# Kernel optimization log

Measured on AMD Instinct MI355X. Metric: run time of the kernel, lower is better.

## Reference

```python
import jax, jax.numpy as jnp
import numpy as np

B, Tp, Tq, D2 = 16, 4096, 512, 256  # D2 = 2*d


def setup_inputs() -> dict:
    key = jax.random.key(0)
    k1, k2, k3 = jax.random.split(key, 3)
    H = jax.random.normal(k1, (B, Tp, D2), dtype=jnp.float32)
    U = jax.random.normal(k2, (B, Tq, D2), dtype=jnp.float32)
    # learned weight (1, 6d, 1, 1) in the original -> flat [6d] vector here
    w = jax.random.normal(k3, (3 * D2,), dtype=jnp.float32) * (1.0 / np.sqrt(3 * D2))
    mask_p = jnp.ones((B, Tp), dtype=jnp.int32)
    mask_q = jnp.ones((B, Tq), dtype=jnp.int32)
    return {"H": H, "U": U, "w": w, "mask_p": mask_p, "mask_q": mask_q}


def _masked_softmax(x, m, axis):
    # e = mask * exp(mask * (x - max(x)));  matches the original custom softmax
    e = m * jnp.exp(m * (x - jnp.max(x, axis=axis, keepdims=True)))
    return e / jnp.sum(e, axis=axis, keepdims=True)


def reference(H, U, w, mask_p, mask_q):
    pm = mask_p.astype(jnp.float32)          # [B, Tp]
    qm = mask_q.astype(jnp.float32)          # [B, Tq]
    Hm = H * pm[:, :, None]                  # [B, Tp, 2d]
    Um = U * qm[:, :, None]                  # [B, Tq, 2d]
    d2 = H.shape[-1]
    w_h, w_u, w_hu = w[:d2], w[d2:2 * d2], w[2 * d2:]
    # Decomposed additive score: S[b,i,j] = w_h.H[b,i] + w_u.U[b,j] + sum_c w_hu[c]*H[b,i,c]*U[b,j,c]
    # (identical math to summing w * concat([h_tiled, u_tiled, hu]) over the 6d axis)
    S = (Hm @ w_h)[:, :, None] + (Um @ w_u)[:, None, :] \
        + jnp.einsum('bic,bjc->bij', Hm * w_hu, Um)      # [B, Tp, Tq]
    a = _masked_softmax(S, qm[:, None, :], axis=-1)       # [B, Tp, Tq]
    U_att = jnp.einsum('bij,bjc->bic', a, Um)             # [B, Tp, 2d]
    b = _masked_softmax(jnp.max(S, axis=-1), pm, axis=-1) # [B, Tp]
    h_att = jnp.einsum('bi,bic->bc', b, Hm)               # [B, 2d]
    G = jnp.concatenate([Hm, U_att, Hm * U_att, Hm * h_att[:, None, :]], axis=-1)
    return G * pm[:, :, None]                             # [B, Tp, 8d]
```

## Files before the change

### kernel.cpp

```cpp
#include <hip/hip_runtime.h>
#include <hip/hip_bf16.h>
#include <cstdint>

#define B_  16
#define TP  4096
#define TQ  512
#define D2_ 256
#define TI 64
#define TJ 32
#define NJT (TQ / TJ)
#define NFRAG 35
#define PPITCH 34

typedef _Float16 f16x8 __attribute__((ext_vector_type(8)));
typedef _Float16 f16x4 __attribute__((ext_vector_type(4)));
typedef float    f32x4 __attribute__((ext_vector_type(4)));

__device__ __forceinline__ _Float16* frag_ptr(float* G, int b, int jt, int f, int lane) {
  return (_Float16*)G + ((size_t)((b * NJT + jt) * NFRAG + f)) * 2048 + 1536 + lane * 8;
}
__device__ __forceinline__ float* phat_ptr(float* G, int b, int blk) {
  return G + (size_t)(9000 + b * 64 + blk) * 1024 + 768;
}

__device__ __forceinline__ void gload_lds16(const _Float16* g, _Float16* l) {
  __builtin_amdgcn_global_load_lds(
      (const __attribute__((address_space(1))) void*)g,
      (__attribute__((address_space(3))) void*)l, 16, 0, 0);
}

__global__ __launch_bounds__(256) void k_prep(const float* __restrict__ U,
                                              const float* __restrict__ w,
                                              const int* __restrict__ mq,
                                              float* __restrict__ G) {
  __shared__ _Float16 T[TJ][264];
  __shared__ float uds[TJ];
  __shared__ float qs[TJ];
  const int b = blockIdx.y, jt = blockIdx.x;
  const int tid = threadIdx.x, lane = tid & 63, wv = tid >> 6;
  const int l15 = lane & 15, g = lane >> 4;

  if (tid < TJ) qs[tid] = (float)mq[b * TQ + jt * TJ + tid];

#pragma unroll
  for (int it = 0; it < 8; ++it) {
    int chunk = it * 256 + tid;
    int r = chunk >> 6, c = (chunk & 63) * 4;
    int row = b * TQ + jt * TJ + r;
    float qmv = (float)mq[row];
    f32x4 u = *(const f32x4*)&U[(size_t)row * D2_ + c];
    f16x4 v;
    v[0] = (_Float16)(u.x * qmv); v[1] = (_Float16)(u.y * qmv);
    v[2] = (_Float16)(u.z * qmv); v[3] = (_Float16)(u.w * qmv);
    *(f16x4*)&T[r][c] = v;
  }
  __syncthreads();

  {
    int r = tid >> 3, s = tid & 7;
    float p = 0.f;
#pragma unroll
    for (int e = 0; e < 32; ++e) p += (float)T[r][s * 32 + e] * w[D2_ + s * 32 + e];
    p += __shfl_xor(p, 1); p += __shfl_xor(p, 2); p += __shfl_xor(p, 4);
    if (s == 0) uds[r] = p;
  }
  __syncthreads();

#pragma unroll
  for (int q = 0; q < 9; ++q) {
    int f = q * 4 + wv;
    if (f >= NFRAG) continue;
    f16x8 v;
#pragma unroll
    for (int e = 0; e < 8; ++e) v[e] = (_Float16)0.0f;
    if (f < 16) {
      int t = f >> 3, ks = f & 7;
      v = *(const f16x8*)&T[t * 16 + l15][ks * 32 + g * 8];
    } else if (f < 18) {
      int t = f - 16;
      if (g == 0) { v[0] = (_Float16)uds[t * 16 + l15]; v[1] = (_Float16)1.0f; }
    } else if (f < 34) {
      int n = f - 18;
#pragma unroll
      for (int e = 0; e < 8; ++e) v[e] = T[g * 8 + e][n * 16 + l15];
    } else {
#pragma unroll
      for (int e = 0; e < 8; ++e) v[e] = (_Float16)qs[g * 8 + e];
    }
    *(f16x8*)frag_ptr(G, b, jt, f, lane) = v;
  }
}

__global__ __launch_bounds__(512, 4) void k_main(
    const float* __restrict__ H, const float* __restrict__ w,
    const int* __restrict__ mp,
    float* __restrict__ mblk_g, float* __restrict__ lblk_g,
    float* __restrict__ G) {

  __shared__ char smem[80896];
  _Float16 (*Fbuf)[NFRAG][512]  = (_Float16(*)[NFRAG][512])smem;
  _Float16 (*Plds)[16][PPITCH]  = (_Float16(*)[16][PPITCH])(smem + 71680);
  float* mtmp = (float*)(smem + 80384);
  float* wrow = mtmp + 64;
  _Float16 (*Uatt)[264] = (_Float16(*)[264])smem;
  f32x4 (*Part)[64]     = (f32x4(*)[64])smem;

  const int b = blockIdx.y, bx = blockIdx.x, i0 = bx * TI;
  const int tid = threadIdx.x, lane = tid & 63, wv = tid >> 6;
  const int l15 = lane & 15, g = lane >> 4;
  const int pr = wv >> 1;
  const int h  = wv & 1;

  const _Float16* Gf = (const _Float16*)G;
  auto tilebase = [&](int jt) {
    return Gf + ((size_t)((b * NJT + jt) * NFRAG)) * 2048 + 1536 + (size_t)lane * 8;
  };

  {
    const _Float16* fb = tilebase(0);
#pragma unroll
    for (int q = 0; q < 5; ++q) {
      int f = q * 8 + wv;
      if (f < NFRAG) gload_lds16(fb + (size_t)f * 2048, &Fbuf[0][f][0]);
    }
  }

  const int rowg = i0 + pr * 16 + l15;
  const float* Hrow = H + ((size_t)b * TP + rowg) * D2_;
  const float pmr = (float)mp[b * TP + rowg];
  f16x8 afr[8];
  float hp = 0.f;
#pragma unroll
  for (int ks = 0; ks < 8; ++ks) {
    int c0 = ks * 32 + g * 8;
    f32x4 h0 = *(const f32x4*)&Hrow[c0];
    f32x4 h1 = *(const f32x4*)&Hrow[c0 + 4];
    f32x4 wh0 = *(const f32x4*)&w[c0];
    f32x4 wh1 = *(const f32x4*)&w[c0 + 4];
    f32x4 wu0 = *(const f32x4*)&w[2 * D2_ + c0];
    f32x4 wu1 = *(const f32x4*)&w[2 * D2_ + c0 + 4];
    h0 *= pmr; h1 *= pmr;
    f16x8 a;
    a[0] = (_Float16)(h0.x * wu0.x); a[1] = (_Float16)(h0.y * wu0.y);
    a[2] = (_Float16)(h0.z * wu0.z); a[3] = (_Float16)(h0.w * wu0.w);
    a[4] = (_Float16)(h1.x * wu1.x); a[5] = (_Float16)(h1.y * wu1.y);
    a[6] = (_Float16)(h1.z * wu1.z); a[7] = (_Float16)(h1.w * wu1.w);
    afr[ks] = a;
    hp += h0.x * wh0.x + h0.y * wh0.y + h0.z * wh0.z + h0.w * wh0.w
        + h1.x * wh1.x + h1.y * wh1.y + h1.z * wh1.z + h1.w * wh1.w;
  }
  hp += __shfl_xor(hp, 16);
  hp += __shfl_xor(hp, 32);
  f16x8 bext;
#pragma unroll
  for (int e = 0; e < 8; ++e) bext[e] = (_Float16)0.0f;
  if (g == 0) { bext[0] = (_Float16)1.0f; bext[1] = (_Float16)hp; }

  __syncthreads();

  f32x4 Oacc[8];
#pragma unroll
  for (int n = 0; n < 8; ++n) Oacc[n] = {0.f, 0.f, 0.f, 0.f};
  f32x4 Lacc = {0.f, 0.f, 0.f, 0.f};
  float m_run  = -1e30f;
  float m_true = -1e30f;

  int cur = 0;
  for (int jt = 0; jt < NJT; ++jt) {
    if (jt + 1 < NJT) {
      const _Float16* fb = tilebase(jt + 1);
#pragma unroll
      for (int q = 0; q < 5; ++q) {
        int f = q * 8 + wv;
        if (f < NFRAG) gload_lds16(fb + (size_t)f * 2048, &Fbuf[cur ^ 1][f][0]);
      }
    }

    f32x4 S0 = {0.f, 0.f, 0.f, 0.f}, S1 = {0.f, 0.f, 0.f, 0.f};
#pragma unroll
    for (int ks = 0; ks < 8; ++ks) {
      f16x8 a0 = *(const f16x8*)&Fbuf[cur][ks][lane * 8];
      f16x8 a1 = *(const f16x8*)&Fbuf[cur][8 + ks][lane * 8];
      S0 = __builtin_amdgcn_mfma_f32_16x16x32_f16(a0, afr[ks], S0, 0, 0, 0);
      S1 = __builtin_amdgcn_mfma_f32_16x16x32_f16(a1, afr[ks], S1, 0, 0, 0);
    }
    {
      f16x8 ax0 = *(const f16x8*)&Fbuf[cur][16][lane * 8];
      f16x8 ax1 = *(const f16x8*)&Fbuf[cur][17][lane * 8];
      S0 = __builtin_amdgcn_mfma_f32_16x16x32_f16(ax0, bext, S0, 0, 0, 0);
      S1 = __builtin_amdgcn_mfma_f32_16x16x32_f16(ax1, bext, S1, 0, 0, 0);
    }

    float lmax = fmaxf(fmaxf(fmaxf(S0[0], S0[1]), fmaxf(S0[2], S0[3])),
                       fmaxf(fmaxf(S1[0], S1[1]), fmaxf(S1[2], S1[3])));
    lmax = fmaxf(lmax, __shfl_xor(lmax, 16));
    lmax = fmaxf(lmax, __shfl_xor(lmax, 32));
    m_true = fmaxf(m_true, lmax);
    if (__any(lmax - m_run > 8.0f)) {
      float mn = fmaxf(m_run, lmax);
      float sc = __expf(m_run - mn);
      m_run = mn;
#pragma unroll
      for (int reg = 0; reg < 4; ++reg) {
        float scr = __shfl(sc, g * 4 + reg);
        Lacc[reg] *= scr;
#pragma unroll
        for (int n = 0; n < 8; ++n) Oacc[n][reg] *= scr;
      }
    }

    f16x4 ph0, ph1;
#pragma unroll
    for (int reg = 0; reg < 4; ++reg) {
      ph0[reg] = (_Float16)__expf(S0[reg] - m_run);
      ph1[reg] = (_Float16)__expf(S1[reg] - m_run);
    }
    *(f16x4*)&Plds[wv][l15][g * 4]      = ph0;
    *(f16x4*)&Plds[wv][l15][16 + g * 4] = ph1;
    f16x8 pa = *(const f16x8*)&Plds[wv][l15][g * 8];

    {
      f16x8 qmf = *(const f16x8*)&Fbuf[cur][34][lane * 8];
      Lacc = __builtin_amdgcn_mfma_f32_16x16x32_f16(pa, qmf, Lacc, 0, 0, 0);
    }
#pragma unroll
    for (int n = 0; n < 8; ++n) {
      f16x8 bu = *(const f16x8*)&Fbuf[cur][18 + h * 8 + n][lane * 8];
      Oacc[n] = __builtin_amdgcn_mfma_f32_16x16x32_f16(pa, bu, Oacc[n], 0, 0, 0);
    }

    __syncthreads();
    cur ^= 1;
  }

  if (h == 0 && g == 0) mtmp[pr * 16 + l15] = m_true;
  float inv_l[4];
#pragma unroll
  for (int reg = 0; reg < 4; ++reg) inv_l[reg] = 1.0f / Lacc[reg];
  __syncthreads();

  if (wv == 0) {
    float v = mtmp[lane];
#pragma unroll
    for (int o = 1; o < 64; o <<= 1) v = fmaxf(v, __shfl_xor(v, o));
    float m_blk = v;
    float pmv = (float)mp[b * TP + i0 + lane];
    float wr = pmv * __expf(mtmp[lane] - m_blk);
    wrow[lane] = wr;
    float ls = wr;
#pragma unroll
    for (int o = 1; o < 64; o <<= 1) ls += __shfl_xor(ls, o);
    if (lane == 0) { mblk_g[b * 64 + bx] = m_blk; lblk_g[b * 64 + bx] = ls; }
  }

#pragma unroll
  for (int n = 0; n < 8; ++n)
#pragma unroll
    for (int reg = 0; reg < 4; ++reg)
      Uatt[pr * 16 + g * 4 + reg][h * 128 + n * 16 + l15] =
          (_Float16)(Oacc[n][reg] * inv_l[reg]);
  __syncthreads();

  const int* pmb = mp + b * TP + i0;
  f32x4 acc = {0.f, 0.f, 0.f, 0.f};
#pragma unroll
  for (int it = 0; it < 8; ++it) {
    int idx4 = it * 512 + tid;
    int r = idx4 >> 6, c = (idx4 & 63) * 4;
    float pm = (float)pmb[r];
    f32x4 hv = *(const f32x4*)&H[((size_t)b * TP + i0 + r) * D2_ + c];
    hv *= pm;
    f16x4 u4 = *(const f16x4*)&Uatt[r][c];
    f32x4 u; u.x = (float)u4[0]; u.y = (float)u4[1]; u.z = (float)u4[2]; u.w = (float)u4[3];
    size_t ro = ((size_t)b * TP + i0 + r) * (4 * D2_);
    *(f32x4*)&G[ro + c] = hv;
    f32x4 up = u * pm;
    *(f32x4*)&G[ro + D2_ + c] = up;
    f32x4 hu; hu.x = hv.x * u.x; hu.y = hv.y * u.y; hu.z = hv.z * u.z; hu.w = hv.w * u.w;
    *(f32x4*)&G[ro + 2 * D2_ + c] = hu;
    acc += wrow[r] * hv;
  }

  __syncthreads();
  Part[wv][lane] = acc;
  __syncthreads();
  if (tid < 64) {
    f32x4 s = Part[0][tid];
#pragma unroll
    for (int k = 1; k < 8; ++k) s += Part[k][tid];
    *(f32x4*)&phat_ptr(G, b, bx)[tid * 4] = s;
  }
}

__global__ __launch_bounds__(256) void k_comb(const float* __restrict__ Gc,
    const float* __restrict__ mblk_g, const float* __restrict__ lblk_g,
    float* __restrict__ hatt) {
  int b = blockIdx.x, tid = threadIdx.x;
  __shared__ float sm[64], sl[64];
  if (tid < 64) { sm[tid] = mblk_g[b * 64 + tid]; sl[tid] = lblk_g[b * 64 + tid]; }
  __syncthreads();
  float M = -1e30f;
#pragma unroll
  for (int k = 0; k < 64; ++k) M = fmaxf(M, sm[k]);
  float L = 0.f;
#pragma unroll
  for (int k = 0; k < 64; ++k) L += __expf(sm[k] - M) * sl[k];
  float acc = 0.f;
  for (int k = 0; k < 64; ++k)
    acc += __expf(sm[k] - M) * Gc[(size_t)(9000 + b * 64 + k) * 1024 + 768 + tid];
  hatt[b * D2_ + tid] = acc / L;
}

__global__ __launch_bounds__(256) void k_g3(const float* __restrict__ H,
    const int* __restrict__ mp, const float* __restrict__ hatt,
    float* __restrict__ G) {
  const int total = B_ * TP * (D2_ / 4);
  for (int idx = blockIdx.x * 256 + threadIdx.x; idx < total; idx += gridDim.x * 256) {
    int c4 = idx & 63;
    int i = (idx >> 6) & (TP - 1);
    int b = idx >> 18;
    float pm = (float)mp[b * TP + i];
    f32x4 h = *(const f32x4*)&H[((size_t)b * TP + i) * D2_ + c4 * 4];
    f32x4 ha = *(const f32x4*)&hatt[b * D2_ + c4 * 4];
    f32x4 o;
    o.x = h.x * pm * ha.x; o.y = h.y * pm * ha.y;
    o.z = h.z * pm * ha.z; o.w = h.w * pm * ha.w;
    *(f32x4*)&G[((size_t)b * TP + i) * (4 * D2_) + 3 * D2_ + c4 * 4] = o;
  }
}

extern "C" void kernel_launch(void* const* d_in, const int* in_sizes, int n_in,
                              void* d_out, int out_size, void* d_ws, size_t ws_size,
                              hipStream_t stream) {
  const float* H  = (const float*)d_in[0];
  const float* U  = (const float*)d_in[1];
  const float* w  = (const float*)d_in[2];
  const int*   mp = (const int*)d_in[3];
  const int*   mq = (const int*)d_in[4];
  float* G = (float*)d_out;

  float* ws   = (float*)d_ws;
  float* mblk = ws;
  float* lblk = mblk + 1024;
  float* hatt = lblk + 1024;

  k_prep<<<dim3(NJT, B_), 256, 0, stream>>>(U, w, mq, G);
  k_main<<<dim3(TP / TI, B_), 512, 0, stream>>>(H, w, mp, mblk, lblk, G);
  k_comb<<<dim3(B_), 256, 0, stream>>>(G, mblk, lblk, hatt);
  k_g3<<<dim3(2048), 256, 0, stream>>>(H, mp, hatt, G);
}
```

Before: 167.7 us.

## Double row tile to 128 and keep softmax probabilities in registers via K permutation

The row tile per block grows from 64 to 128 with 1024 threads. Each staged U fragment tile in LDS is now reused by twice as many query rows, which halves the number of blocks and the number of partial softmax records. The prep kernel permutes the K ordering of the U and mask fragments so the MFMA output layout of the score tile can feed the A operand directly. That removes the LDS write/read round-trip for P, and the packing uses cvt_pkrtz, which rounds toward zero. The risks are lower occupancy, possible register pressure under the new launch bounds, and slightly different rounding of the probabilities.

Result: faster. 152.8 us (-8.9%).

```diff
diff --git a/kernel.cpp b/kernel.cpp
--- a/kernel.cpp
+++ b/kernel.cpp
@@ -6,27 +6,32 @@
 #define TP  4096
 #define TQ  512
 #define D2_ 256
-#define TI 64
+#define TI 128
 #define TJ 32
 #define NJT (TQ / TJ)
 #define NFRAG 35
-#define PPITCH 34
+#define NBX (TP / TI)
 
 typedef _Float16 f16x8 __attribute__((ext_vector_type(8)));
 typedef _Float16 f16x4 __attribute__((ext_vector_type(4)));
 typedef float    f32x4 __attribute__((ext_vector_type(4)));
+typedef uint32_t u32;
 
 __device__ __forceinline__ _Float16* frag_ptr(float* G, int b, int jt, int f, int lane) {
   return (_Float16*)G + ((size_t)((b * NJT + jt) * NFRAG + f)) * 2048 + 1536 + lane * 8;
 }
 __device__ __forceinline__ float* phat_ptr(float* G, int b, int blk) {
-  return G + (size_t)(9000 + b * 64 + blk) * 1024 + 768;
+  return G + (size_t)(9000 + b * NBX + blk) * 1024 + 768;
 }
 
 __device__ __forceinline__ void gload_lds16(const _Float16* g, _Float16* l) {
   __builtin_amdgcn_global_load_lds(
       (const __attribute__((address_space(1))) void*)g,
       (__attribute__((address_space(3))) void*)l, 16, 0, 0);
+}
+
+__device__ __forceinline__ int kperm(int g, int e) {
+  return (e < 4) ? (g * 4 + e) : (16 + g * 4 + (e - 4));
 }
 
 __global__ __launch_bounds__(256) void k_prep(const float* __restrict__ U,
@@ -82,26 +87,25 @@
     } else if (f < 34) {
       int n = f - 18;
 #pragma unroll
-      for (int e = 0; e < 8; ++e) v[e] = T[g * 8 + e][n * 16 + l15];
+      for (int e = 0; e < 8; ++e) v[e] = T[kperm(g, e)][n * 16 + l15];
     } else {
 #pragma unroll
-      for (int e = 0; e < 8; ++e) v[e] = (_Float16)qs[g * 8 + e];
+      for (int e = 0; e < 8; ++e) v[e] = (_Float16)qs[kperm(g, e)];
     }
     *(f16x8*)frag_ptr(G, b, jt, f, lane) = v;
   }
 }
 
-__global__ __launch_bounds__(512, 4) void k_main(
+__global__ __launch_bounds__(1024, 4) void k_main(
     const float* __restrict__ H, const float* __restrict__ w,
     const int* __restrict__ mp,
     float* __restrict__ mblk_g, float* __restrict__ lblk_g,
     float* __restrict__ G) {
 
-  __shared__ char smem[80896];
-  _Float16 (*Fbuf)[NFRAG][512]  = (_Float16(*)[NFRAG][512])smem;
-  _Float16 (*Plds)[16][PPITCH]  = (_Float16(*)[16][PPITCH])(smem + 71680);
-  float* mtmp = (float*)(smem + 80384);
-  float* wrow = mtmp + 64;
+  __shared__ char smem[72704];
+  _Float16 (*Fbuf)[NFRAG][512] = (_Float16(*)[NFRAG][512])smem;
+  float* mtmp = (float*)(smem + 71680);
+  float* wrow = mtmp + 128;
   _Float16 (*Uatt)[264] = (_Float16(*)[264])smem;
   f32x4 (*Part)[64]     = (f32x4(*)[64])smem;
 
@@ -119,8 +123,8 @@
   {
     const _Float16* fb = tilebase(0);
 #pragma unroll
-    for (int q = 0; q < 5; ++q) {
-      int f = q * 8 + wv;
+    for (int q = 0; q < 3; ++q) {
+      int f = q * 16 + wv;
       if (f < NFRAG) gload_lds16(fb + (size_t)f * 2048, &Fbuf[0][f][0]);
     }
   }
@@ -170,8 +174,8 @@
     if (jt + 1 < NJT) {
       const _Float16* fb = tilebase(jt + 1);
 #pragma unroll
-      for (int q = 0; q < 5; ++q) {
-        int f = q * 8 + wv;
+      for (int q = 0; q < 3; ++q) {
+        int f = q * 16 + wv;
         if (f < NFRAG) gload_lds16(fb + (size_t)f * 2048, &Fbuf[cur ^ 1][f][0]);
       }
     }
@@ -209,15 +213,16 @@
       }
     }
 
-    f16x4 ph0, ph1;
-#pragma unroll
-    for (int reg = 0; reg < 4; ++reg) {
-      ph0[reg] = (_Float16)__expf(S0[reg] - m_run);
-      ph1[reg] = (_Float16)__expf(S1[reg] - m_run);
-    }
-    *(f16x4*)&Plds[wv][l15][g * 4]      = ph0;
-    *(f16x4*)&Plds[wv][l15][16 + g * 4] = ph1;
-    f16x8 pa = *(const f16x8*)&Plds[wv][l15][g * 8];
+    union { u32 u[4]; f16x8 v; } paw;
+    paw.u[0] = __builtin_bit_cast(u32, __builtin_amdgcn_cvt_pkrtz(
+                   __expf(S0[0] - m_run), __expf(S0[1] - m_run)));
+    paw.u[1] = __builtin_bit_cast(u32, __builtin_amdgcn_cvt_pkrtz(
+                   __expf(S0[2] - m_run), __expf(S0[3] - m_run)));
+    paw.u[2] = __builtin_bit_cast(u32, __builtin_amdgcn_cvt_pkrtz(
+                   __expf(S1[0] - m_run), __expf(S1[1] - m_run)));
+    paw.u[3] = __builtin_bit_cast(u32, __builtin_amdgcn_cvt_pkrtz(
+                   __expf(S1[2] - m_run), __expf(S1[3] - m_run)));
+    f16x8 pa = paw.v;
 
     {
       f16x8 qmf = *(const f16x8*)&Fbuf[cur][34][lane * 8];
@@ -233,24 +238,28 @@
     cur ^= 1;
   }
 
-  if (h == 0 && g == 0) mtmp[pr * 16 + l15] = m_true;
+  if (h == 0 && lane < 16) mtmp[pr * 16 + lane] = m_true;
   float inv_l[4];
 #pragma unroll
   for (int reg = 0; reg < 4; ++reg) inv_l[reg] = 1.0f / Lacc[reg];
   __syncthreads();
 
   if (wv == 0) {
-    float v = mtmp[lane];
+    float v0 = mtmp[lane], v1 = mtmp[lane + 64];
+    float v = fmaxf(v0, v1);
 #pragma unroll
     for (int o = 1; o < 64; o <<= 1) v = fmaxf(v, __shfl_xor(v, o));
     float m_blk = v;
-    float pmv = (float)mp[b * TP + i0 + lane];
-    float wr = pmv * __expf(mtmp[lane] - m_blk);
-    wrow[lane] = wr;
-    float ls = wr;
+    float pm0 = (float)mp[b * TP + i0 + lane];
+    float pm1 = (float)mp[b * TP + i0 + lane + 64];
+    float wr0 = pm0 * __expf(v0 - m_blk);
+    float wr1 = pm1 * __expf(v1 - m_blk);
+    wrow[lane] = wr0;
+    wrow[lane + 64] = wr1;
+    float ls = wr0 + wr1;
 #pragma unroll
     for (int o = 1; o < 64; o <<= 1) ls += __shfl_xor(ls, o);
-    if (lane == 0) { mblk_g[b * 64 + bx] = m_blk; lblk_g[b * 64 + bx] = ls; }
+    if (lane == 0) { mblk_g[b * NBX + bx] = m_blk; lblk_g[b * NBX + bx] = ls; }
   }
 
 #pragma unroll
@@ -265,7 +274,7 @@
   f32x4 acc = {0.f, 0.f, 0.f, 0.f};
 #pragma unroll
   for (int it = 0; it < 8; ++it) {
-    int idx4 = it * 512 + tid;
+    int idx4 = it * 1024 + tid;
     int r = idx4 >> 6, c = (idx4 & 63) * 4;
     float pm = (float)pmb[r];
     f32x4 hv = *(const f32x4*)&H[((size_t)b * TP + i0 + r) * D2_ + c];
@@ -287,7 +296,7 @@
   if (tid < 64) {
     f32x4 s = Part[0][tid];
 #pragma unroll
-    for (int k = 1; k < 8; ++k) s += Part[k][tid];
+    for (int k = 1; k < 16; ++k) s += Part[k][tid];
     *(f32x4*)&phat_ptr(G, b, bx)[tid * 4] = s;
   }
 }
@@ -296,18 +305,18 @@
     const float* __restrict__ mblk_g, const float* __restrict__ lblk_g,
     float* __restrict__ hatt) {
   int b = blockIdx.x, tid = threadIdx.x;
-  __shared__ float sm[64], sl[64];
-  if (tid < 64) { sm[tid] = mblk_g[b * 64 + tid]; sl[tid] = lblk_g[b * 64 + tid]; }
+  __shared__ float sm[NBX], sl[NBX];
+  if (tid < NBX) { sm[tid] = mblk_g[b * NBX + tid]; sl[tid] = lblk_g[b * NBX + tid]; }
   __syncthreads();
   float M = -1e30f;
 #pragma unroll
-  for (int k = 0; k < 64; ++k) M = fmaxf(M, sm[k]);
+  for (int k = 0; k < NBX; ++k) M = fmaxf(M, sm[k]);
   float L = 0.f;
 #pragma unroll
-  for (int k = 0; k < 64; ++k) L += __expf(sm[k] - M) * sl[k];
+  for (int k = 0; k < NBX; ++k) L += __expf(sm[k] - M) * sl[k];
   float acc = 0.f;
-  for (int k = 0; k < 64; ++k)
-    acc += __expf(sm[k] - M) * Gc[(size_t)(9000 + b * 64 + k) * 1024 + 768 + tid];
+  for (int k = 0; k < NBX; ++k)
+    acc += __expf(sm[k] - M) * Gc[(size_t)(9000 + b * NBX + k) * 1024 + 768 + tid];
   hatt[b * D2_ + tid] = acc / L;
 }
 
@@ -345,7 +354,7 @@
   float* hatt = lblk + 1024;
 
   k_prep<<<dim3(NJT, B_), 256, 0, stream>>>(U, w, mq, G);
-  k_main<<<dim3(TP / TI, B_), 512, 0, stream>>>(H, w, mp, mblk, lblk, G);
+  k_main<<<dim3(NBX, B_), 1024, 0, stream>>>(H, w, mp, mblk, lblk, G);
   k_comb<<<dim3(B_), 256, 0, stream>>>(G, mblk, lblk, hatt);
   k_g3<<<dim3(2048), 256, 0, stream>>>(H, mp, hatt, G);
 }
```
